# Performance work log

Measured on AMD Instinct MI355X. Metric: run time of the kernel, lower is better.

The kernel has to match this reference:

```python
import jax, jax.numpy as jnp
import numpy as np

HIDDEN = 4096
K = 4          # Gibbs sampling steps
LR = 0.01
IMG = (16, 64, 64, 3)  # batch, H, W, C


def setup_inputs() -> dict:
    key = jax.random.key(0)
    k1, k2 = jax.random.split(key)
    inputs = jax.random.uniform(k1, IMG, dtype=jnp.float32)
    flat = IMG[1] * IMG[2] * IMG[3]
    # GlorotNormal init: std = sqrt(2 / (fan_in + fan_out))
    scale = (2.0 / (flat + HIDDEN)) ** 0.5
    W = jax.random.normal(k2, (flat, HIDDEN), dtype=jnp.float32) * scale
    a = jnp.zeros((flat, 1), dtype=jnp.float32)
    b = jnp.zeros((HIDDEN, 1), dtype=jnp.float32)
    return {"inputs": inputs, "W": W, "a": a, "b": b}


def reference(inputs, W, a, b):
    B = inputs.shape[0]
    flat = inputs.shape[1] * inputs.shape[2] * inputs.shape[3]
    vs = inputs.reshape(B, flat, 1)  # each sample is a (flat,1) column vector

    def per_sample(carry, v):
        W, a, b = carry
        v_init = v
        # k Gibbs steps: h = sigma(b + W^T v); v = sigma(a + W h)
        h = None
        for _ in range(K):
            h = jax.nn.sigmoid(b + W.T @ v)
            v = jax.nn.sigmoid(a + W @ h)
        h_init = jax.nn.sigmoid(b + W.T @ v_init)
        # Contrastive divergence with .assign (replace, not accumulate) as in source
        W_new = LR * (v_init @ h_init.T - v @ h.T)
        a_new = LR * (v_init - v)
        b_new = LR * (h_init - h)
        return (W_new, a_new, b_new), v

    _, vs_out = jax.lax.scan(per_sample, (W, a, b), vs)
    # call() returns self.v, i.e. the reconstruction of the LAST batch element
    return vs_out[-1]
```

## Files before the change

kernel.cpp:

```cpp
#include <hip/hip_runtime.h>
#include <math.h>

#define FLAT 12288
#define NH   4096
#define KSTEPS 4
#define LRC 0.01f
#define NSEG 384
#define RPS  32
#define WSCALE 64.0f
#define WINV   0.015625f

typedef float v2f __attribute__((ext_vector_type(2)));

__device__ __forceinline__ float sigm(float x) {
    return __builtin_amdgcn_rcpf(1.0f + __expf(-x));
}

template <int CTRL>
__device__ __forceinline__ float dpp_add(float x) {
    int s = __builtin_amdgcn_update_dpp(0, __float_as_int(x), CTRL, 0xf, 0xf, true);
    return x + __int_as_float(s);
}
__device__ __forceinline__ float wave_sum63(float x) {
    x = dpp_add<0x111>(x);
    x = dpp_add<0x112>(x);
    x = dpp_add<0x114>(x);
    x = dpp_add<0x118>(x);
    x = dpp_add<0x142>(x);
    x = dpp_add<0x143>(x);
    return x;
}


__global__ __launch_bounds__(256) void k_colpart_cvt(const float* __restrict__ W,
                                                     const float* __restrict__ v,
                                                     float* __restrict__ partials,
                                                     unsigned int* __restrict__ W8) {
    const float4* W4 = (const float4*)W;
    int c4 = blockIdx.x * 256 + threadIdx.x;
    int r0 = blockIdx.y * RPS;
    float4 acc = make_float4(0.f, 0.f, 0.f, 0.f);
    for (int r = r0; r < r0 + RPS; ++r) {
        float vr = v[r];
        float4 w = W4[(size_t)r * (NH / 4) + c4];
        acc.x = fmaf(w.x, vr, acc.x);
        acc.y = fmaf(w.y, vr, acc.y);
        acc.z = fmaf(w.z, vr, acc.z);
        acc.w = fmaf(w.w, vr, acc.w);
        unsigned int p = 0;
        p = __builtin_amdgcn_cvt_pk_fp8_f32(w.x * WSCALE, w.y * WSCALE, p, false);
        p = __builtin_amdgcn_cvt_pk_fp8_f32(w.z * WSCALE, w.w * WSCALE, p, true);
        W8[(size_t)r * (NH / 4) + c4] = p;
    }
    ((float4*)partials)[(size_t)blockIdx.y * (NH / 4) + c4] = acc;
}

__global__ __launch_bounds__(256) void k_colpart_fp8(const uint4* __restrict__ W8,
                                                     const float* __restrict__ v,
                                                     float* __restrict__ partials) {
    int c16 = threadIdx.x;
    int r0 = blockIdx.x * RPS;
    float acc[16];
#pragma unroll
    for (int i = 0; i < 16; i++) acc[i] = 0.f;
    for (int r = r0; r < r0 + RPS; ++r) {
        float vr = v[r] * WINV;
        uint4 w = W8[(size_t)r * (NH / 16) + c16];
        v2f f;
        f = __builtin_amdgcn_cvt_pk_f32_fp8(w.x, false); acc[0]  = fmaf(f.x, vr, acc[0]);  acc[1]  = fmaf(f.y, vr, acc[1]);
        f = __builtin_amdgcn_cvt_pk_f32_fp8(w.x, true);  acc[2]  = fmaf(f.x, vr, acc[2]);  acc[3]  = fmaf(f.y, vr, acc[3]);
        f = __builtin_amdgcn_cvt_pk_f32_fp8(w.y, false); acc[4]  = fmaf(f.x, vr, acc[4]);  acc[5]  = fmaf(f.y, vr, acc[5]);
        f = __builtin_amdgcn_cvt_pk_f32_fp8(w.y, true);  acc[6]  = fmaf(f.x, vr, acc[6]);  acc[7]  = fmaf(f.y, vr, acc[7]);
        f = __builtin_amdgcn_cvt_pk_f32_fp8(w.z, false); acc[8]  = fmaf(f.x, vr, acc[8]);  acc[9]  = fmaf(f.y, vr, acc[9]);
        f = __builtin_amdgcn_cvt_pk_f32_fp8(w.z, true);  acc[10] = fmaf(f.x, vr, acc[10]); acc[11] = fmaf(f.y, vr, acc[11]);
        f = __builtin_amdgcn_cvt_pk_f32_fp8(w.w, false); acc[12] = fmaf(f.x, vr, acc[12]); acc[13] = fmaf(f.y, vr, acc[13]);
        f = __builtin_amdgcn_cvt_pk_f32_fp8(w.w, true);  acc[14] = fmaf(f.x, vr, acc[14]); acc[15] = fmaf(f.y, vr, acc[15]);
    }
    float4* P = (float4*)(partials + (size_t)blockIdx.x * NH + (size_t)c16 * 16);
#pragma unroll
    for (int q = 0; q < 4; q++) {
        float4 o; o.x = acc[4*q]; o.y = acc[4*q+1]; o.z = acc[4*q+2]; o.w = acc[4*q+3];
        P[q] = o;
    }
}

__global__ __launch_bounds__(256) void k_hreduce(const float* __restrict__ partials,
                                                 const float* __restrict__ b,
                                                 float* __restrict__ h,
                                                 float* __restrict__ hi,
                                                 int nseg) {
    int c  = threadIdx.x & 31;
    int sg = threadIdx.x >> 5;
    int col = blockIdx.x * 32 + c;
    float s = 0.f;
    for (int g = sg; g < nseg; g += 8) s += partials[(size_t)g * NH + col];
    __shared__ float red[8][33];
    red[sg][c] = s;
    __syncthreads();
    if (threadIdx.x < 32) {
        float t = 0.f;
#pragma unroll
        for (int g2 = 0; g2 < 8; g2++) t += red[g2][threadIdx.x];
        float hh = sigm(t + b[col]);
        h[col] = hh;
        if (hi) hi[col] = hh;
    }
}

__global__ __launch_bounds__(256) void k_vstep_fp8(const unsigned char* __restrict__ W8,
                                                   const float* __restrict__ h,
                                                   const float* __restrict__ a,
                                                   float* __restrict__ v) {
    int wid = threadIdx.x >> 6, lane = threadIdx.x & 63;
    int row = blockIdx.x * 4 + wid;
    const uint4* Wr = (const uint4*)(W8 + (size_t)row * NH);
    const float4* h4 = (const float4*)h;
    float acc = 0.f;
    for (int k = lane; k < NH / 16; k += 64) {
        uint4 w = Wr[k];
        float4 h0 = h4[4*k], h1 = h4[4*k+1], h2 = h4[4*k+2], h3 = h4[4*k+3];
        v2f f;
        f = __builtin_amdgcn_cvt_pk_f32_fp8(w.x, false); acc = fmaf(f.x, h0.x, acc); acc = fmaf(f.y, h0.y, acc);
        f = __builtin_amdgcn_cvt_pk_f32_fp8(w.x, true);  acc = fmaf(f.x, h0.z, acc); acc = fmaf(f.y, h0.w, acc);
        f = __builtin_amdgcn_cvt_pk_f32_fp8(w.y, false); acc = fmaf(f.x, h1.x, acc); acc = fmaf(f.y, h1.y, acc);
        f = __builtin_amdgcn_cvt_pk_f32_fp8(w.y, true);  acc = fmaf(f.x, h1.z, acc); acc = fmaf(f.y, h1.w, acc);
        f = __builtin_amdgcn_cvt_pk_f32_fp8(w.z, false); acc = fmaf(f.x, h2.x, acc); acc = fmaf(f.y, h2.y, acc);
        f = __builtin_amdgcn_cvt_pk_f32_fp8(w.z, true);  acc = fmaf(f.x, h2.z, acc); acc = fmaf(f.y, h2.w, acc);
        f = __builtin_amdgcn_cvt_pk_f32_fp8(w.w, false); acc = fmaf(f.x, h3.x, acc); acc = fmaf(f.y, h3.y, acc);
        f = __builtin_amdgcn_cvt_pk_f32_fp8(w.w, true);  acc = fmaf(f.x, h3.z, acc); acc = fmaf(f.y, h3.w, acc);
    }
    acc = wave_sum63(acc);
    if (lane == 63) v[row] = sigm(a[row] + acc * WINV);
}


#define TB  512
#define RVB (FLAT / TB)
#define RHB (NH / TB)
#define NWAVES (TB / 64)

__global__ __launch_bounds__(512) void k_phaseB(const float* __restrict__ inputs,
                                                const float* __restrict__ hi0,
                                                const float* __restrict__ hk0,
                                                const float* __restrict__ vk0,
                                                float* __restrict__ out) {
    int t = threadIdx.x;
    int lane = t & 63, wid = t >> 6;
    __shared__ float2 red[2][NWAVES];

    float Vi[RVB], Vk[RVB], v[RVB], Vn[RVB];
    float Hi[RHB], Hk[RHB], h[RHB], hini[RHB];

#pragma unroll
    for (int r = 0; r < RVB; r++) { int i = r * TB + t; Vi[r] = inputs[i]; Vk[r] = vk0[i]; }
#pragma unroll
    for (int r = 0; r < RHB; r++) { int j = r * TB + t; Hi[r] = hi0[j]; Hk[r] = hk0[j]; }

    int rc = 0;
    for (int s = 1; s < 16; ++s) {
        const float* vin = inputs + (size_t)s * FLAT;
#pragma unroll
        for (int r = 0; r < RVB; r++) { Vn[r] = vin[r * TB + t]; v[r] = Vn[r]; }

        for (int k = 0; k < KSTEPS; ++k) {
            float px0 = 0.f, px1 = 0.f, px2 = 0.f, px3 = 0.f;
            float py0 = 0.f, py1 = 0.f, py2 = 0.f, py3 = 0.f;
#pragma unroll
            for (int r = 0; r < RVB; r += 4) {
                px0 = fmaf(Vi[r],   v[r],   px0); py0 = fmaf(Vk[r],   v[r],   py0);
                px1 = fmaf(Vi[r+1], v[r+1], px1); py1 = fmaf(Vk[r+1], v[r+1], py1);
                px2 = fmaf(Vi[r+2], v[r+2], px2); py2 = fmaf(Vk[r+2], v[r+2], py2);
                px3 = fmaf(Vi[r+3], v[r+3], px3); py3 = fmaf(Vk[r+3], v[r+3], py3);
            }
            float px = wave_sum63((px0 + px1) + (px2 + px3));
            float py = wave_sum63((py0 + py1) + (py2 + py3));
            if (lane == 63) { float2 w2; w2.x = px; w2.y = py; red[rc & 1][wid] = w2; }
            __syncthreads();
            float al, be;
            {
                const float4* R4 = (const float4*)&red[rc & 1][0];
                float4 r0 = R4[0], r1 = R4[1], r2 = R4[2], r3 = R4[3];
                al = (r0.x + r1.x) + (r2.x + r3.x) + ((r0.z + r1.z) + (r2.z + r3.z));
                be = (r0.y + r1.y) + (r2.y + r3.y) + ((r0.w + r1.w) + (r2.w + r3.w));
            }
            rc++;
            float ca = LRC * (1.f + al), cb = LRC * (1.f + be);

            float qx0 = 0.f, qx1 = 0.f, qy0 = 0.f, qy1 = 0.f;
#pragma unroll
            for (int r = 0; r < RHB; r += 2) {
                float h0 = sigm(ca * Hi[r]   - cb * Hk[r]);
                float h1 = sigm(ca * Hi[r+1] - cb * Hk[r+1]);
                h[r] = h0; h[r+1] = h1;
                if (k == 0) { hini[r] = h0; hini[r+1] = h1; }
                qx0 = fmaf(Hi[r],   h0, qx0); qy0 = fmaf(Hk[r],   h0, qy0);
                qx1 = fmaf(Hi[r+1], h1, qx1); qy1 = fmaf(Hk[r+1], h1, qy1);
            }
            float qx = wave_sum63(qx0 + qx1), qy = wave_sum63(qy0 + qy1);
            if (lane == 63) { float2 w2; w2.x = qx; w2.y = qy; red[rc & 1][wid] = w2; }
            __syncthreads();
            float ga, de;
            {
                const float4* R4 = (const float4*)&red[rc & 1][0];
                float4 r0 = R4[0], r1 = R4[1], r2 = R4[2], r3 = R4[3];
                ga = (r0.x + r1.x) + (r2.x + r3.x) + ((r0.z + r1.z) + (r2.z + r3.z));
                de = (r0.y + r1.y) + (r2.y + r3.y) + ((r0.w + r1.w) + (r2.w + r3.w));
            }
            rc++;
            float cg = LRC * (1.f + ga), cd = LRC * (1.f + de);

#pragma unroll
            for (int r = 0; r < RVB; r++) v[r] = sigm(cg * Vi[r] - cd * Vk[r]);
        }

#pragma unroll
        for (int r = 0; r < RVB; r++) { Vk[r] = v[r]; Vi[r] = Vn[r]; }
#pragma unroll
        for (int r = 0; r < RHB; r++) { Hk[r] = h[r]; Hi[r] = hini[r]; }
    }

#pragma unroll
    for (int r = 0; r < RVB; r++) out[r * TB + t] = Vk[r];
}


extern "C" void kernel_launch(void* const* d_in, const int* in_sizes, int n_in,
                              void* d_out, int out_size, void* d_ws, size_t ws_size,
                              hipStream_t stream) {
    const float* inputs = (const float*)d_in[0];
    const float* W      = (const float*)d_in[1];
    const float* a_in   = (const float*)d_in[2];
    const float* b_in   = (const float*)d_in[3];
    float* out = (float*)d_out;

    unsigned int* W8 = (unsigned int*)d_ws;
    float* partials = (float*)((char*)d_ws + (size_t)FLAT * NH);
    float* h  = partials + (size_t)NSEG * NH;
    float* hi = h + NH;
    float* v  = hi + NH;

    dim3 blk(256);

    k_colpart_cvt<<<dim3(4, NSEG), blk, 0, stream>>>(W, inputs, partials, W8);
    k_hreduce<<<dim3(NH / 32), blk, 0, stream>>>(partials, b_in, h, hi, NSEG);
    k_vstep_fp8<<<dim3(FLAT / 4), blk, 0, stream>>>((const unsigned char*)W8, h, a_in, v);

    for (int k = 1; k < KSTEPS; ++k) {
        k_colpart_fp8<<<dim3(NSEG), blk, 0, stream>>>((const uint4*)W8, v, partials);
        k_hreduce<<<dim3(NH / 32), blk, 0, stream>>>(partials, b_in, h, (float*)nullptr, NSEG);
        k_vstep_fp8<<<dim3(FLAT / 4), blk, 0, stream>>>((const unsigned char*)W8, h, a_in, v);
    }

    k_phaseB<<<1, TB, 0, stream>>>(inputs, hi, h, v, out);
}
```

Measured before the change: 537.5 us.

## Fuse v-step and next h partial matvec into one pass over FP8 weights

```diff
diff --git a/kernel.cpp b/kernel.cpp
--- a/kernel.cpp
+++ b/kernel.cpp
@@ -7,6 +7,7 @@
 #define LRC 0.01f
 #define NSEG 384
 #define RPS  32
+#define NSEGF 2048
 #define WSCALE 64.0f
 #define WINV   0.015625f
 
@@ -29,6 +30,38 @@
     x = dpp_add<0x142>(x);
     x = dpp_add<0x143>(x);
     return x;
+}
+
+__device__ __forceinline__ float dot64(const uint4* wq, const float4* hreg) {
+    float d0 = 0.f, d1 = 0.f, d2 = 0.f, d3 = 0.f;
+#pragma unroll
+    for (int j = 0; j < 4; j++) {
+        v2f f;
+        f = __builtin_amdgcn_cvt_pk_f32_fp8(wq[j].x, false); d0 = fmaf(f.x, hreg[4*j+0].x, d0); d1 = fmaf(f.y, hreg[4*j+0].y, d1);
+        f = __builtin_amdgcn_cvt_pk_f32_fp8(wq[j].x, true);  d2 = fmaf(f.x, hreg[4*j+0].z, d2); d3 = fmaf(f.y, hreg[4*j+0].w, d3);
+        f = __builtin_amdgcn_cvt_pk_f32_fp8(wq[j].y, false); d0 = fmaf(f.x, hreg[4*j+1].x, d0); d1 = fmaf(f.y, hreg[4*j+1].y, d1);
+        f = __builtin_amdgcn_cvt_pk_f32_fp8(wq[j].y, true);  d2 = fmaf(f.x, hreg[4*j+1].z, d2); d3 = fmaf(f.y, hreg[4*j+1].w, d3);
+        f = __builtin_amdgcn_cvt_pk_f32_fp8(wq[j].z, false); d0 = fmaf(f.x, hreg[4*j+2].x, d0); d1 = fmaf(f.y, hreg[4*j+2].y, d1);
+        f = __builtin_amdgcn_cvt_pk_f32_fp8(wq[j].z, true);  d2 = fmaf(f.x, hreg[4*j+2].z, d2); d3 = fmaf(f.y, hreg[4*j+2].w, d3);
+        f = __builtin_amdgcn_cvt_pk_f32_fp8(wq[j].w, false); d0 = fmaf(f.x, hreg[4*j+3].x, d0); d1 = fmaf(f.y, hreg[4*j+3].y, d1);
+        f = __builtin_amdgcn_cvt_pk_f32_fp8(wq[j].w, true);  d2 = fmaf(f.x, hreg[4*j+3].z, d2); d3 = fmaf(f.y, hreg[4*j+3].w, d3);
+    }
+    return (d0 + d1) + (d2 + d3);
+}
+
+__device__ __forceinline__ void pacc64(const uint4* wq, float vs, float* pacc) {
+#pragma unroll
+    for (int j = 0; j < 4; j++) {
+        v2f f;
+        f = __builtin_amdgcn_cvt_pk_f32_fp8(wq[j].x, false); pacc[16*j+0]  = fmaf(f.x, vs, pacc[16*j+0]);  pacc[16*j+1]  = fmaf(f.y, vs, pacc[16*j+1]);
+        f = __builtin_amdgcn_cvt_pk_f32_fp8(wq[j].x, true);  pacc[16*j+2]  = fmaf(f.x, vs, pacc[16*j+2]);  pacc[16*j+3]  = fmaf(f.y, vs, pacc[16*j+3]);
+        f = __builtin_amdgcn_cvt_pk_f32_fp8(wq[j].y, false); pacc[16*j+4]  = fmaf(f.x, vs, pacc[16*j+4]);  pacc[16*j+5]  = fmaf(f.y, vs, pacc[16*j+5]);
+        f = __builtin_amdgcn_cvt_pk_f32_fp8(wq[j].y, true);  pacc[16*j+6]  = fmaf(f.x, vs, pacc[16*j+6]);  pacc[16*j+7]  = fmaf(f.y, vs, pacc[16*j+7]);
+        f = __builtin_amdgcn_cvt_pk_f32_fp8(wq[j].z, false); pacc[16*j+8]  = fmaf(f.x, vs, pacc[16*j+8]);  pacc[16*j+9]  = fmaf(f.y, vs, pacc[16*j+9]);
+        f = __builtin_amdgcn_cvt_pk_f32_fp8(wq[j].z, true);  pacc[16*j+10] = fmaf(f.x, vs, pacc[16*j+10]); pacc[16*j+11] = fmaf(f.y, vs, pacc[16*j+11]);
+        f = __builtin_amdgcn_cvt_pk_f32_fp8(wq[j].w, false); pacc[16*j+12] = fmaf(f.x, vs, pacc[16*j+12]); pacc[16*j+13] = fmaf(f.y, vs, pacc[16*j+13]);
+        f = __builtin_amdgcn_cvt_pk_f32_fp8(wq[j].w, true);  pacc[16*j+14] = fmaf(f.x, vs, pacc[16*j+14]); pacc[16*j+15] = fmaf(f.y, vs, pacc[16*j+15]);
+    }
 }
 
 
@@ -55,35 +88,6 @@
     ((float4*)partials)[(size_t)blockIdx.y * (NH / 4) + c4] = acc;
 }
 
-__global__ __launch_bounds__(256) void k_colpart_fp8(const uint4* __restrict__ W8,
-                                                     const float* __restrict__ v,
-                                                     float* __restrict__ partials) {
-    int c16 = threadIdx.x;
-    int r0 = blockIdx.x * RPS;
-    float acc[16];
-#pragma unroll
-    for (int i = 0; i < 16; i++) acc[i] = 0.f;
-    for (int r = r0; r < r0 + RPS; ++r) {
-        float vr = v[r] * WINV;
-        uint4 w = W8[(size_t)r * (NH / 16) + c16];
-        v2f f;
-        f = __builtin_amdgcn_cvt_pk_f32_fp8(w.x, false); acc[0]  = fmaf(f.x, vr, acc[0]);  acc[1]  = fmaf(f.y, vr, acc[1]);
-        f = __builtin_amdgcn_cvt_pk_f32_fp8(w.x, true);  acc[2]  = fmaf(f.x, vr, acc[2]);  acc[3]  = fmaf(f.y, vr, acc[3]);
-        f = __builtin_amdgcn_cvt_pk_f32_fp8(w.y, false); acc[4]  = fmaf(f.x, vr, acc[4]);  acc[5]  = fmaf(f.y, vr, acc[5]);
-        f = __builtin_amdgcn_cvt_pk_f32_fp8(w.y, true);  acc[6]  = fmaf(f.x, vr, acc[6]);  acc[7]  = fmaf(f.y, vr, acc[7]);
-        f = __builtin_amdgcn_cvt_pk_f32_fp8(w.z, false); acc[8]  = fmaf(f.x, vr, acc[8]);  acc[9]  = fmaf(f.y, vr, acc[9]);
-        f = __builtin_amdgcn_cvt_pk_f32_fp8(w.z, true);  acc[10] = fmaf(f.x, vr, acc[10]); acc[11] = fmaf(f.y, vr, acc[11]);
-        f = __builtin_amdgcn_cvt_pk_f32_fp8(w.w, false); acc[12] = fmaf(f.x, vr, acc[12]); acc[13] = fmaf(f.y, vr, acc[13]);
-        f = __builtin_amdgcn_cvt_pk_f32_fp8(w.w, true);  acc[14] = fmaf(f.x, vr, acc[14]); acc[15] = fmaf(f.y, vr, acc[15]);
-    }
-    float4* P = (float4*)(partials + (size_t)blockIdx.x * NH + (size_t)c16 * 16);
-#pragma unroll
-    for (int q = 0; q < 4; q++) {
-        float4 o; o.x = acc[4*q]; o.y = acc[4*q+1]; o.z = acc[4*q+2]; o.w = acc[4*q+3];
-        P[q] = o;
-    }
-}
-
 __global__ __launch_bounds__(256) void k_hreduce(const float* __restrict__ partials,
                                                  const float* __restrict__ b,
                                                  float* __restrict__ h,
@@ -104,6 +108,51 @@
         float hh = sigm(t + b[col]);
         h[col] = hh;
         if (hi) hi[col] = hh;
+    }
+}
+
+__global__ __launch_bounds__(512) void k_fused(const uint4* __restrict__ W84,
+                                               const float* __restrict__ h,
+                                               const float* __restrict__ a,
+                                               float* __restrict__ v,
+                                               float* __restrict__ partials) {
+    const int lane = threadIdx.x & 63, wv = threadIdx.x >> 6;
+    const float4* h4 = (const float4*)h;
+
+    float4 hreg[16];
+#pragma unroll
+    for (int j = 0; j < 4; j++)
+#pragma unroll
+        for (int q = 0; q < 4; q++) hreg[4*j+q] = h4[4 * (lane + 64*j) + q];
+
+    float pacc[64];
+#pragma unroll
+    for (int i = 0; i < 64; i++) pacc[i] = 0.f;
+
+    const int rbase = blockIdx.x * 48 + wv * 6;
+    for (int i = 0; i < 6; ++i) {
+        int r = rbase + i;
+        uint4 wq[4];
+#pragma unroll
+        for (int j = 0; j < 4; j++) wq[j] = W84[(size_t)r * 256 + lane + 64*j];
+        float d = wave_sum63(dot64(wq, hreg));
+        float full = __shfl(d, 63);
+        float vr = sigm(a[r] + full * WINV);
+        if (lane == 63) v[r] = vr;
+        pacc64(wq, vr * WINV, pacc);
+    }
+
+    float* P = partials + (size_t)(blockIdx.x * 8 + wv) * NH;
+#pragma unroll
+    for (int j = 0; j < 4; j++) {
+        float4* Pj = (float4*)(P + 16 * (lane + 64*j));
+#pragma unroll
+        for (int q = 0; q < 4; q++) {
+            float4 o;
+            o.x = pacc[16*j + 4*q + 0]; o.y = pacc[16*j + 4*q + 1];
+            o.z = pacc[16*j + 4*q + 2]; o.w = pacc[16*j + 4*q + 3];
+            Pj[q] = o;
+        }
     }
 }
 
@@ -235,7 +284,7 @@
 
     unsigned int* W8 = (unsigned int*)d_ws;
     float* partials = (float*)((char*)d_ws + (size_t)FLAT * NH);
-    float* h  = partials + (size_t)NSEG * NH;
+    float* h  = partials + (size_t)NSEGF * NH;
     float* hi = h + NH;
     float* v  = hi + NH;
 
@@ -243,13 +292,12 @@
 
     k_colpart_cvt<<<dim3(4, NSEG), blk, 0, stream>>>(W, inputs, partials, W8);
     k_hreduce<<<dim3(NH / 32), blk, 0, stream>>>(partials, b_in, h, hi, NSEG);
+
+    for (int k = 1; k < KSTEPS; ++k) {
+        k_fused<<<dim3(256), dim3(512), 0, stream>>>((const uint4*)W8, h, a_in, v, partials);
+        k_hreduce<<<dim3(NH / 32), blk, 0, stream>>>(partials, b_in, h, (float*)nullptr, NSEGF);
+    }
     k_vstep_fp8<<<dim3(FLAT / 4), blk, 0, stream>>>((const unsigned char*)W8, h, a_in, v);
 
-    for (int k = 1; k < KSTEPS; ++k) {
-        k_colpart_fp8<<<dim3(NSEG), blk, 0, stream>>>((const uint4*)W8, v, partials);
-        k_hreduce<<<dim3(NH / 32), blk, 0, stream>>>(partials, b_in, h, (float*)nullptr, NSEG);
-        k_vstep_fp8<<<dim3(FLAT / 4), blk, 0, stream>>>((const unsigned char*)W8, h, a_in, v);
-    }
-
     k_phaseB<<<1, TB, 0, stream>>>(inputs, hi, h, v, out);
 }
```

Result: slower. 667.0 us (+24.1%).

## Replace partial-sum reduction kernel with atomics and fuse sigmoid into v-step

Applied to the files above, without the earlier changes.

```diff
diff --git a/kernel.cpp b/kernel.cpp
--- a/kernel.cpp
+++ b/kernel.cpp
@@ -7,6 +7,8 @@
 #define LRC 0.01f
 #define NSEG 384
 #define RPS  32
+#define NB2  192
+#define RPS2 64
 #define WSCALE 64.0f
 #define WINV   0.015625f
 
@@ -14,6 +16,12 @@
 
 __device__ __forceinline__ float sigm(float x) {
     return __builtin_amdgcn_rcpf(1.0f + __expf(-x));
+}
+__device__ __forceinline__ float4 sigm4(float4 x, float4 b) {
+    float4 o;
+    o.x = sigm(x.x + b.x); o.y = sigm(x.y + b.y);
+    o.z = sigm(x.z + b.z); o.w = sigm(x.w + b.w);
+    return o;
 }
 
 template <int CTRL>
@@ -31,10 +39,31 @@
     return x;
 }
 
+__device__ __forceinline__ float dot64(const uint4* wq, const float4* hreg) {
+    float d0 = 0.f, d1 = 0.f, d2 = 0.f, d3 = 0.f;
+#pragma unroll
+    for (int j = 0; j < 4; j++) {
+        v2f f;
+        f = __builtin_amdgcn_cvt_pk_f32_fp8(wq[j].x, false); d0 = fmaf(f.x, hreg[4*j+0].x, d0); d1 = fmaf(f.y, hreg[4*j+0].y, d1);
+        f = __builtin_amdgcn_cvt_pk_f32_fp8(wq[j].x, true);  d2 = fmaf(f.x, hreg[4*j+0].z, d2); d3 = fmaf(f.y, hreg[4*j+0].w, d3);
+        f = __builtin_amdgcn_cvt_pk_f32_fp8(wq[j].y, false); d0 = fmaf(f.x, hreg[4*j+1].x, d0); d1 = fmaf(f.y, hreg[4*j+1].y, d1);
+        f = __builtin_amdgcn_cvt_pk_f32_fp8(wq[j].y, true);  d2 = fmaf(f.x, hreg[4*j+1].z, d2); d3 = fmaf(f.y, hreg[4*j+1].w, d3);
+        f = __builtin_amdgcn_cvt_pk_f32_fp8(wq[j].z, false); d0 = fmaf(f.x, hreg[4*j+2].x, d0); d1 = fmaf(f.y, hreg[4*j+2].y, d1);
+        f = __builtin_amdgcn_cvt_pk_f32_fp8(wq[j].z, true);  d2 = fmaf(f.x, hreg[4*j+2].z, d2); d3 = fmaf(f.y, hreg[4*j+2].w, d3);
+        f = __builtin_amdgcn_cvt_pk_f32_fp8(wq[j].w, false); d0 = fmaf(f.x, hreg[4*j+3].x, d0); d1 = fmaf(f.y, hreg[4*j+3].y, d1);
+        f = __builtin_amdgcn_cvt_pk_f32_fp8(wq[j].w, true);  d2 = fmaf(f.x, hreg[4*j+3].z, d2); d3 = fmaf(f.y, hreg[4*j+3].w, d3);
+    }
+    return (d0 + d1) + (d2 + d3);
+}
+
+
+__global__ __launch_bounds__(256) void k_zero(float4* __restrict__ p) {
+    p[blockIdx.x * 256 + threadIdx.x] = make_float4(0.f, 0.f, 0.f, 0.f);
+}
 
 __global__ __launch_bounds__(256) void k_colpart_cvt(const float* __restrict__ W,
                                                      const float* __restrict__ v,
-                                                     float* __restrict__ partials,
+                                                     float* __restrict__ hpre,
                                                      unsigned int* __restrict__ W8) {
     const float4* W4 = (const float4*)W;
     int c4 = blockIdx.x * 256 + threadIdx.x;
@@ -52,18 +81,22 @@
         p = __builtin_amdgcn_cvt_pk_fp8_f32(w.z * WSCALE, w.w * WSCALE, p, true);
         W8[(size_t)r * (NH / 4) + c4] = p;
     }
-    ((float4*)partials)[(size_t)blockIdx.y * (NH / 4) + c4] = acc;
+    int c = c4 * 4;
+    atomicAdd(&hpre[c],     acc.x);
+    atomicAdd(&hpre[c + 1], acc.y);
+    atomicAdd(&hpre[c + 2], acc.z);
+    atomicAdd(&hpre[c + 3], acc.w);
 }
 
 __global__ __launch_bounds__(256) void k_colpart_fp8(const uint4* __restrict__ W8,
                                                      const float* __restrict__ v,
-                                                     float* __restrict__ partials) {
+                                                     float* __restrict__ hpre) {
     int c16 = threadIdx.x;
-    int r0 = blockIdx.x * RPS;
+    int r0 = blockIdx.x * RPS2;
     float acc[16];
 #pragma unroll
     for (int i = 0; i < 16; i++) acc[i] = 0.f;
-    for (int r = r0; r < r0 + RPS; ++r) {
+    for (int r = r0; r < r0 + RPS2; ++r) {
         float vr = v[r] * WINV;
         uint4 w = W8[(size_t)r * (NH / 16) + c16];
         v2f f;
@@ -76,60 +109,35 @@
         f = __builtin_amdgcn_cvt_pk_f32_fp8(w.w, false); acc[12] = fmaf(f.x, vr, acc[12]); acc[13] = fmaf(f.y, vr, acc[13]);
         f = __builtin_amdgcn_cvt_pk_f32_fp8(w.w, true);  acc[14] = fmaf(f.x, vr, acc[14]); acc[15] = fmaf(f.y, vr, acc[15]);
     }
-    float4* P = (float4*)(partials + (size_t)blockIdx.x * NH + (size_t)c16 * 16);
-#pragma unroll
-    for (int q = 0; q < 4; q++) {
-        float4 o; o.x = acc[4*q]; o.y = acc[4*q+1]; o.z = acc[4*q+2]; o.w = acc[4*q+3];
-        P[q] = o;
-    }
-}
-
-__global__ __launch_bounds__(256) void k_hreduce(const float* __restrict__ partials,
-                                                 const float* __restrict__ b,
-                                                 float* __restrict__ h,
-                                                 float* __restrict__ hi,
-                                                 int nseg) {
-    int c  = threadIdx.x & 31;
-    int sg = threadIdx.x >> 5;
-    int col = blockIdx.x * 32 + c;
-    float s = 0.f;
-    for (int g = sg; g < nseg; g += 8) s += partials[(size_t)g * NH + col];
-    __shared__ float red[8][33];
-    red[sg][c] = s;
-    __syncthreads();
-    if (threadIdx.x < 32) {
-        float t = 0.f;
-#pragma unroll
-        for (int g2 = 0; g2 < 8; g2++) t += red[g2][threadIdx.x];
-        float hh = sigm(t + b[col]);
-        h[col] = hh;
-        if (hi) hi[col] = hh;
-    }
-}
-
-__global__ __launch_bounds__(256) void k_vstep_fp8(const unsigned char* __restrict__ W8,
-                                                   const float* __restrict__ h,
+    float* H = hpre + c16 * 16;
+#pragma unroll
+    for (int i = 0; i < 16; i++) atomicAdd(&H[i], acc[i]);
+}
+
+__global__ __launch_bounds__(256) void k_vstep_act(const uint4* __restrict__ W84,
+                                                   const float* __restrict__ hpre,
+                                                   const float* __restrict__ bb,
                                                    const float* __restrict__ a,
                                                    float* __restrict__ v) {
     int wid = threadIdx.x >> 6, lane = threadIdx.x & 63;
     int row = blockIdx.x * 4 + wid;
-    const uint4* Wr = (const uint4*)(W8 + (size_t)row * NH);
-    const float4* h4 = (const float4*)h;
-    float acc = 0.f;
-    for (int k = lane; k < NH / 16; k += 64) {
-        uint4 w = Wr[k];
-        float4 h0 = h4[4*k], h1 = h4[4*k+1], h2 = h4[4*k+2], h3 = h4[4*k+3];
-        v2f f;
-        f = __builtin_amdgcn_cvt_pk_f32_fp8(w.x, false); acc = fmaf(f.x, h0.x, acc); acc = fmaf(f.y, h0.y, acc);
-        f = __builtin_amdgcn_cvt_pk_f32_fp8(w.x, true);  acc = fmaf(f.x, h0.z, acc); acc = fmaf(f.y, h0.w, acc);
-        f = __builtin_amdgcn_cvt_pk_f32_fp8(w.y, false); acc = fmaf(f.x, h1.x, acc); acc = fmaf(f.y, h1.y, acc);
-        f = __builtin_amdgcn_cvt_pk_f32_fp8(w.y, true);  acc = fmaf(f.x, h1.z, acc); acc = fmaf(f.y, h1.w, acc);
-        f = __builtin_amdgcn_cvt_pk_f32_fp8(w.z, false); acc = fmaf(f.x, h2.x, acc); acc = fmaf(f.y, h2.y, acc);
-        f = __builtin_amdgcn_cvt_pk_f32_fp8(w.z, true);  acc = fmaf(f.x, h2.z, acc); acc = fmaf(f.y, h2.w, acc);
-        f = __builtin_amdgcn_cvt_pk_f32_fp8(w.w, false); acc = fmaf(f.x, h3.x, acc); acc = fmaf(f.y, h3.y, acc);
-        f = __builtin_amdgcn_cvt_pk_f32_fp8(w.w, true);  acc = fmaf(f.x, h3.z, acc); acc = fmaf(f.y, h3.w, acc);
-    }
-    acc = wave_sum63(acc);
+    const float4* hp4 = (const float4*)hpre;
+    const float4* b4  = (const float4*)bb;
+
+    float4 hreg[16];
+#pragma unroll
+    for (int j = 0; j < 4; j++) {
+#pragma unroll
+        for (int q = 0; q < 4; q++) {
+            int idx = 4 * (lane + 64 * j) + q;
+            hreg[4 * j + q] = sigm4(hp4[idx], b4[idx]);
+        }
+    }
+
+    uint4 wq[4];
+#pragma unroll
+    for (int j = 0; j < 4; j++) wq[j] = W84[(size_t)row * 256 + lane + 64 * j];
+    float acc = wave_sum63(dot64(wq, hreg));
     if (lane == 63) v[row] = sigm(a[row] + acc * WINV);
 }
 
@@ -140,8 +148,9 @@
 #define NWAVES (TB / 64)
 
 __global__ __launch_bounds__(512) void k_phaseB(const float* __restrict__ inputs,
-                                                const float* __restrict__ hi0,
-                                                const float* __restrict__ hk0,
+                                                const float* __restrict__ hpre0,
+                                                const float* __restrict__ hpreL,
+                                                const float* __restrict__ bb,
                                                 const float* __restrict__ vk0,
                                                 float* __restrict__ out) {
     int t = threadIdx.x;
@@ -154,7 +163,12 @@
 #pragma unroll
     for (int r = 0; r < RVB; r++) { int i = r * TB + t; Vi[r] = inputs[i]; Vk[r] = vk0[i]; }
 #pragma unroll
-    for (int r = 0; r < RHB; r++) { int j = r * TB + t; Hi[r] = hi0[j]; Hk[r] = hk0[j]; }
+    for (int r = 0; r < RHB; r++) {
+        int j = r * TB + t;
+        float bj = bb[j];
+        Hi[r] = sigm(hpre0[j] + bj);
+        Hk[r] = sigm(hpreL[j] + bj);
+    }
 
     int rc = 0;
     for (int s = 1; s < 16; ++s) {
@@ -234,22 +248,26 @@
     float* out = (float*)d_out;
 
     unsigned int* W8 = (unsigned int*)d_ws;
-    float* partials = (float*)((char*)d_ws + (size_t)FLAT * NH);
-    float* h  = partials + (size_t)NSEG * NH;
-    float* hi = h + NH;
-    float* v  = hi + NH;
+    float* hp = (float*)((char*)d_ws + (size_t)FLAT * NH);
+    float* hp0 = hp;
+    float* hp1 = hp + NH;
+    float* hp2 = hp + 2 * NH;
+    float* hp3 = hp + 3 * NH;
+    float* v   = hp + 4 * NH;
 
     dim3 blk(256);
 
-    k_colpart_cvt<<<dim3(4, NSEG), blk, 0, stream>>>(W, inputs, partials, W8);
-    k_hreduce<<<dim3(NH / 32), blk, 0, stream>>>(partials, b_in, h, hi, NSEG);
-    k_vstep_fp8<<<dim3(FLAT / 4), blk, 0, stream>>>((const unsigned char*)W8, h, a_in, v);
-
-    for (int k = 1; k < KSTEPS; ++k) {
-        k_colpart_fp8<<<dim3(NSEG), blk, 0, stream>>>((const uint4*)W8, v, partials);
-        k_hreduce<<<dim3(NH / 32), blk, 0, stream>>>(partials, b_in, h, (float*)nullptr, NSEG);
-        k_vstep_fp8<<<dim3(FLAT / 4), blk, 0, stream>>>((const unsigned char*)W8, h, a_in, v);
-    }
-
-    k_phaseB<<<1, TB, 0, stream>>>(inputs, hi, h, v, out);
-}
+    k_zero<<<dim3(16), blk, 0, stream>>>((float4*)hp);
+
+    k_colpart_cvt<<<dim3(4, NSEG), blk, 0, stream>>>(W, inputs, hp0, W8);
+    k_vstep_act<<<dim3(FLAT / 4), blk, 0, stream>>>((const uint4*)W8, hp0, b_in, a_in, v);
+
+    k_colpart_fp8<<<dim3(NB2), blk, 0, stream>>>((const uint4*)W8, v, hp1);
+    k_vstep_act<<<dim3(FLAT / 4), blk, 0, stream>>>((const uint4*)W8, hp1, b_in, a_in, v);
+    k_colpart_fp8<<<dim3(NB2), blk, 0, stream>>>((const uint4*)W8, v, hp2);
+    k_vstep_act<<<dim3(FLAT / 4), blk, 0, stream>>>((const uint4*)W8, hp2, b_in, a_in, v);
+    k_colpart_fp8<<<dim3(NB2), blk, 0, stream>>>((const uint4*)W8, v, hp3);
+    k_vstep_act<<<dim3(FLAT / 4), blk, 0, stream>>>((const uint4*)W8, hp3, b_in, a_in, v);
+
+    k_phaseB<<<1, dim3(TB), 0, stream>>>(inputs, hp0, hp3, b_in, v, out);
+}
```

Result: slower. 825.3 us (+53.5%).
